# Kernel tuning notes

Hardware: AMD Instinct MI355X
Metric: run time of the kernel (lower is better)

Reference implementation:

```python
import jax, jax.numpy as jnp
import numpy as np

H = 8
HD = 16  # head_dim = out_features // n_heads = 128 // 8


def setup_inputs() -> dict:
    key = jax.random.key(0)
    k1, k2, k3, k4, k5 = jax.random.split(key, 5)
    B, N, F_IN, F_OUT = 4, 2048, 128, 128
    x = jax.random.normal(k1, (B, N, F_IN), dtype=jnp.float32)
    adj = jax.random.randint(k2, (B, N, N), 0, 2, dtype=jnp.int32)
    W = jax.random.normal(k3, (F_IN, F_OUT), dtype=jnp.float32) * (1.0 / np.sqrt(F_IN))
    a = jax.random.normal(k4, (H, 2 * HD), dtype=jnp.float32) * 0.1
    Wo = jax.random.normal(k5, (F_OUT, F_OUT), dtype=jnp.float32) * (1.0 / np.sqrt(F_OUT))
    bo = jnp.zeros((F_OUT,), dtype=jnp.float32)
    return {"x": x, "adj": adj, "W": W, "a": a, "Wo": Wo, "bo": bo}


def reference(x, adj, W, a, Wo, bo):
    B, N, _ = x.shape
    # Linear projection (no bias), split heads: [B,H,N,HD]
    Wx = (x @ W).reshape(B, N, H, HD).transpose(0, 2, 1, 3)
    # Additive attention scores: e_ij = leaky(a_l . Wx_i + a_r . Wx_j)
    e_i = jnp.einsum('bhnd,hd->bhn', Wx, a[:, :HD])  # [B,H,N]
    e_j = jnp.einsum('bhnd,hd->bhn', Wx, a[:, HD:])  # [B,H,N]
    e = jax.nn.leaky_relu(e_i[:, :, :, None] + e_j[:, :, None, :], negative_slope=0.2)
    # Mask to edges of adj; rows with no edges -> all -inf -> softmax NaN -> 0
    mask = (adj[:, None, :, :] == 0)  # [B,1,N,N] broadcast over heads
    e = jnp.where(mask, -jnp.inf, e)
    attn = jax.nn.softmax(e, axis=-1)
    attn = jnp.nan_to_num(attn, nan=0.0)
    # Weighted aggregation, merge heads: [B,N,F_OUT]
    h = jnp.einsum('bhij,bhjd->bhid', attn, Wx)
    h = h.transpose(0, 2, 1, 3).reshape(B, N, H * HD)
    # out_proj (nn.Linear: y = h @ Wo.T + bo) then ELU
    return jax.nn.elu(h @ Wo.T + bo)
```

## Files before the change

### kernel.cpp

```cpp
#include <hip/hip_runtime.h>
#include <hip/hip_bf16.h>
#include <cstdint>


typedef float f32x2 __attribute__((ext_vector_type(2)));
typedef float f32x4 __attribute__((ext_vector_type(4)));
typedef __bf16 bf16x8 __attribute__((ext_vector_type(8)));
typedef unsigned long long u64;

__device__ __forceinline__ float lsel(float v, u64 m, u64 lanebit) {
#if __has_builtin(__builtin_amdgcn_inverse_ballot_w64)
    (void)lanebit;
    return __builtin_amdgcn_inverse_ballot_w64(m) ? v : 0.0f;
#else
    return (m & lanebit) ? v : 0.0f;
#endif
}

__global__ __launch_bounds__(256)
void prep_kernel(const float* __restrict__ x, const float* __restrict__ W,
                 const float* __restrict__ a, const float* __restrict__ Wo,
                 const int* __restrict__ adj,
                 unsigned short* __restrict__ wxT,
                 float2* __restrict__ EI,
                 float* __restrict__ EjT, float* __restrict__ Ej5T,
                 float* __restrict__ WoT,
                 u64* __restrict__ tmask)
{
    const int t = threadIdx.x;

    if (blockIdx.x < 2048) {
        __shared__ int al[16][257];
        const int blk2 = blockIdx.x;
        const int b = blk2 >> 9;
        const int tile = (blk2 >> 2) & 127;
        const int jq = blk2 & 3;
        const int rowbase = b * 2048 + tile * 16;
        const int w = t >> 6, lane = t & 63;
        const int r = lane & 15, jg = lane >> 4;
        const int srow = t >> 4, scol = (t & 15) * 16;

        #pragma unroll
        for (int cc = 0; cc < 2; ++cc) {
            const int jc = jq * 512 + cc * 256;
            const int* gsrc = adj + (size_t)(rowbase + srow) * 2048 + jc + scol;
            #pragma unroll
            for (int q = 0; q < 4; ++q) {
                const int4 v = *reinterpret_cast<const int4*>(&gsrc[q * 4]);
                al[srow][scol + q * 4 + 0] = v.x;
                al[srow][scol + q * 4 + 1] = v.y;
                al[srow][scol + q * 4 + 2] = v.z;
                al[srow][scol + q * 4 + 3] = v.w;
            }
            __syncthreads();
            u64 myw = 0;
            #pragma unroll
            for (int kk = 0; kk < 2; ++kk) {
                const int c0 = w * 64 + kk * 32 + jg * 8;
                const int4 a0 = *reinterpret_cast<const int4*>(&al[r][c0]);
                const int4 a1 = *reinterpret_cast<const int4*>(&al[r][c0 + 4]);
                const int av[8] = {a0.x, a0.y, a0.z, a0.w, a1.x, a1.y, a1.z, a1.w};
                #pragma unroll
                for (int e = 0; e < 8; ++e) {
                    const u64 bal = __ballot(av[e] != 0);
                    const int widx = kk * 8 + e;
                    if (lane == widx) myw = bal;
                }
            }
            __syncthreads();
            const int jtw = jq * 8 + cc * 4 + w;
            if (lane < 16)
                tmask[((size_t)(b * 128 + tile) * 32 + jtw) * 16 + lane] = myw;
        }
        return;
    }

    const int blk = blockIdx.x - 2048;
    if (blk == 1024) {
        if (t < 128)
            for (int k = 0; k < 128; ++k)
                WoT[k * 128 + t] = Wo[t * 128 + k];
        return;
    }
    __shared__ float xl[8 * 128];
    __shared__ float xw[8 * 128];
    const int row0 = blk * 8;
    if (t < 128) {
        #pragma unroll
        for (int r = 0; r < 8; ++r)
            xl[r * 128 + t] = x[(size_t)(row0 + r) * 128 + t];
    }
    __syncthreads();

    if (t < 128) {
        float acc[8] = {0.f, 0.f, 0.f, 0.f, 0.f, 0.f, 0.f, 0.f};
        for (int k = 0; k < 128; k += 4) {
            const float w0 = W[(k + 0) * 128 + t];
            const float w1 = W[(k + 1) * 128 + t];
            const float w2 = W[(k + 2) * 128 + t];
            const float w3 = W[(k + 3) * 128 + t];
            #pragma unroll
            for (int r = 0; r < 8; ++r) {
                const float4 xv = *reinterpret_cast<const float4*>(&xl[r * 128 + k]);
                acc[r] += xv.x * w0 + xv.y * w1 + xv.z * w2 + xv.w * w3;
            }
        }
        #pragma unroll
        for (int r = 0; r < 8; ++r) xw[r * 128 + t] = acc[r];
    }
    __syncthreads();

    if (t < 128) {
        const int b = row0 >> 11, n0 = row0 & 2047;
        bf16x8 st;
        #pragma unroll
        for (int r = 0; r < 8; ++r) st[r] = (__bf16)xw[r * 128 + t];
        *reinterpret_cast<bf16x8*>(&wxT[((size_t)(b * 128 + t)) * 2048 + n0]) = st;

        const int r = t >> 4, h = (t >> 1) & 7, s = t & 1;
        float dot = 0.f;
        #pragma unroll
        for (int d = 0; d < 16; ++d)
            dot += xw[r * 128 + h * 16 + d] * a[h * 32 + s * 16 + d];
        const float ef  = __expf(dot);
        const float ef5 = __expf(0.2f * dot);
        const int idx = (b * 8 + h) * 2048 + n0 + r;
        if (s) { EjT[idx] = ef; Ej5T[idx] = ef5; }
        else   { float2 ev; ev.x = ef; ev.y = ef5; EI[idx] = ev; }
    }
}

__global__ __launch_bounds__(256)
void vshuf_kernel(const unsigned short* __restrict__ wxT,
                  unsigned short* __restrict__ vfrag)
{
    const int gid = blockIdx.x * 256 + threadIdx.x;
    const int lane = gid & 63;
    const int w32 = (gid >> 6) & 63;
    const int bh = gid >> 12;
    const int b = bh >> 3, h = bh & 7;
    const int f = h * 16 + (lane & 15);
    const int j = w32 * 32 + (lane >> 4) * 8;
    const bf16x8 v = *reinterpret_cast<const bf16x8*>(
        &wxT[((size_t)(b * 128 + f)) * 2048 + j]);
    *reinterpret_cast<bf16x8*>(&vfrag[(size_t)gid * 8]) = v;
}

__global__ __launch_bounds__(512, 4)
void gat_kernel(const u64* __restrict__ tmask,
                const unsigned short* __restrict__ vfrag,
                const float2* __restrict__ EI,
                const float* __restrict__ EjT, const float* __restrict__ Ej5T,
                const float* __restrict__ WoT, const float* __restrict__ bo,
                float* __restrict__ out)
{
    const int tid = threadIdx.x;
    const int h = tid >> 6;
    const int lane = tid & 63;
    const int r = lane & 15;
    const int jg = lane >> 4;
    const int jaof = jg * 8;
    const u64 lanebit = 1ull << lane;
    const int bid = (blockIdx.x & 7) * 64 + (blockIdx.x >> 3);
    const int b = bid >> 7;
    const int tile = bid & 127;
    const int ibase = tile << 4;

    __shared__ __align__(16) float EjL[2][8][128];
    __shared__ __align__(16) float Ej5L[2][8][128];
    __shared__ float hacc[16][128];

    const int eb = (b * 8 + h) * 2048;
    const float2 q0 = EI[eb + ibase + r];
    f32x2 EiE, Ei5E;
    EiE[0] = q0.x; EiE[1] = q0.x; Ei5E[0] = q0.y; Ei5E[1] = q0.y;
    const u64* tmrow = tmask + (size_t)(b * 128 + tile) * 512;

    const unsigned short* vfr = vfrag + (size_t)(b * 8 + h) * 64 * 64 * 8;
    const int jj = lane;
    const float* EjG  = EjT  + eb;
    const float* Ej5G = Ej5T + eb;

    f32x4 acc  = {0.f, 0.f, 0.f, 0.f};
    f32x4 accS = {0.f, 0.f, 0.f, 0.f};
    bf16x8 ones;
    #pragma unroll
    for (int e2 = 0; e2 < 8; ++e2) ones[e2] = (__bf16)1.0f;

    bf16x8 vC0, vC1, vC2, vC3, vN0, vN1, vN2, vN3;
    vC0 = *reinterpret_cast<const bf16x8*>(&vfr[(0 * 64 + lane) * 8]);
    vC1 = *reinterpret_cast<const bf16x8*>(&vfr[(1 * 64 + lane) * 8]);
    vC2 = *reinterpret_cast<const bf16x8*>(&vfr[(2 * 64 + lane) * 8]);
    vC3 = *reinterpret_cast<const bf16x8*>(&vfr[(3 * 64 + lane) * 8]);
    {
        const float2 s0 = *reinterpret_cast<const float2*>(&EjG[jj * 2]);
        const float2 s1 = *reinterpret_cast<const float2*>(&Ej5G[jj * 2]);
        *reinterpret_cast<float2*>(&EjL[0][h][jj * 2]) = s0;
        *reinterpret_cast<float2*>(&Ej5L[0][h][jj * 2]) = s1;
    }
    __syncthreads();

    int cur = 0;
    for (int c = 0; c < 16; ++c) {
        const int cn = (c + 1) & 15;
        const int w32n = cn * 4;
        const int jn = (c + 1) * 128;
        vN0 = *reinterpret_cast<const bf16x8*>(&vfr[((w32n + 0) * 64 + lane) * 8]);
        vN1 = *reinterpret_cast<const bf16x8*>(&vfr[((w32n + 1) * 64 + lane) * 8]);
        vN2 = *reinterpret_cast<const bf16x8*>(&vfr[((w32n + 2) * 64 + lane) * 8]);
        vN3 = *reinterpret_cast<const bf16x8*>(&vfr[((w32n + 3) * 64 + lane) * 8]);
        const float2 sn  = *reinterpret_cast<const float2*>(&EjG[jn + jj * 2]);
        const float2 sn5 = *reinterpret_cast<const float2*>(&Ej5G[jn + jj * 2]);
        __builtin_amdgcn_sched_barrier(0);

        const u64* tmw = tmrow + c * 32;
        u64 mwA[16], mwB[16];
        #pragma unroll
        for (int e2 = 0; e2 < 16; ++e2) mwA[e2] = tmw[e2];
        #pragma unroll
        for (int e2 = 0; e2 < 16; ++e2) mwB[e2] = tmw[16 + e2];

        #pragma unroll
        for (int kk = 0; kk < 4; ++kk) {
            const int jloc = kk * 32 + jaof;
            const float4 e0 = *reinterpret_cast<const float4*>(&EjL[cur][h][jloc]);
            const float4 e1 = *reinterpret_cast<const float4*>(&EjL[cur][h][jloc + 4]);
            const float4 f0 = *reinterpret_cast<const float4*>(&Ej5L[cur][h][jloc]);
            const float4 f1 = *reinterpret_cast<const float4*>(&Ej5L[cur][h][jloc + 4]);
            const bf16x8 v = (kk == 0) ? vC0 : (kk == 1) ? vC1 : (kk == 2) ? vC2 : vC3;
            const u64* mwp = (kk < 2) ? mwA : mwB;
            const int mof = (kk & 1) * 8;
            bf16x8 afr;
            #pragma unroll
            for (int ep = 0; ep < 4; ++ep) {
                const float4 ejv = (ep & 2) ? e1 : e0;
                const float4 ej5 = (ep & 2) ? f1 : f0;
                f32x2 ejp, ej5p;
                if (ep & 1) { ejp[0]=ejv.z; ejp[1]=ejv.w; ej5p[0]=ej5.z; ej5p[1]=ej5.w; }
                else        { ejp[0]=ejv.x; ejp[1]=ejv.y; ej5p[0]=ej5.x; ej5p[1]=ej5.y; }
                const f32x2 t1 = EiE * ejp;
                const f32x2 t2 = Ei5E * ej5p;
#if __has_builtin(__builtin_elementwise_max)
                const f32x2 tm2 = __builtin_elementwise_max(t1, t2);
#else
                f32x2 tm2; tm2[0] = fmaxf(t1[0], t2[0]); tm2[1] = fmaxf(t1[1], t2[1]);
#endif
                afr[2 * ep]     = (__bf16)lsel(tm2[0], mwp[mof + 2 * ep],     lanebit);
                afr[2 * ep + 1] = (__bf16)lsel(tm2[1], mwp[mof + 2 * ep + 1], lanebit);
            }
            acc  = __builtin_amdgcn_mfma_f32_16x16x32_bf16(afr, v,    acc,  0, 0, 0);
            accS = __builtin_amdgcn_mfma_f32_16x16x32_bf16(afr, ones, accS, 0, 0, 0);
        }

        const int nb = cur ^ 1;
        *reinterpret_cast<float2*>(&EjL[nb][h][jj * 2]) = sn;
        *reinterpret_cast<float2*>(&Ej5L[nb][h][jj * 2]) = sn5;
        __syncthreads();
        vC0 = vN0; vC1 = vN1; vC2 = vN2; vC3 = vN3;
        cur = nb;
    }

    #pragma unroll
    for (int q = 0; q < 4; ++q) {
        const int row = jg * 4 + q;
        const float inv = (accS[q] > 0.f) ? 1.f / accS[q] : 0.f;
        hacc[row][h * 16 + r] = acc[q] * inv;
    }
    __syncthreads();

    const int f = tid & 127;
    const int rg = tid >> 7;
    float o0 = 0.f, o1 = 0.f, o2 = 0.f, o3 = 0.f;
    for (int k = 0; k < 128; k += 4) {
        const float w0 = WoT[(k + 0) * 128 + f];
        const float w1 = WoT[(k + 1) * 128 + f];
        const float w2 = WoT[(k + 2) * 128 + f];
        const float w3 = WoT[(k + 3) * 128 + f];
        const float4 h0 = *reinterpret_cast<const float4*>(&hacc[rg * 4 + 0][k]);
        const float4 h1 = *reinterpret_cast<const float4*>(&hacc[rg * 4 + 1][k]);
        const float4 h2v = *reinterpret_cast<const float4*>(&hacc[rg * 4 + 2][k]);
        const float4 h3 = *reinterpret_cast<const float4*>(&hacc[rg * 4 + 3][k]);
        o0 += h0.x * w0 + h0.y * w1 + h0.z * w2 + h0.w * w3;
        o1 += h1.x * w0 + h1.y * w1 + h1.z * w2 + h1.w * w3;
        o2 += h2v.x * w0 + h2v.y * w1 + h2v.z * w2 + h2v.w * w3;
        o3 += h3.x * w0 + h3.y * w1 + h3.z * w2 + h3.w * w3;
    }
    const float bv = bo[f];
    float vv[4] = {o0 + bv, o1 + bv, o2 + bv, o3 + bv};
    #pragma unroll
    for (int q = 0; q < 4; ++q) {
        float v = vv[q];
        v = (v > 0.f) ? v : (__expf(v) - 1.f);
        out[(size_t)(b * 2048 + ibase + rg * 4 + q) * 128 + f] = v;
    }
}

extern "C" void kernel_launch(void* const* d_in, const int* in_sizes, int n_in,
                              void* d_out, int out_size, void* d_ws, size_t ws_size,
                              hipStream_t stream) {
    const float* x   = (const float*)d_in[0];
    const int*   adj = (const int*)d_in[1];
    const float* W   = (const float*)d_in[2];
    const float* a   = (const float*)d_in[3];
    const float* Wo  = (const float*)d_in[4];
    const float* bo  = (const float*)d_in[5];
    float* out = (float*)d_out;

    char* ws = (char*)d_ws;
    unsigned short* wxT = (unsigned short*)ws;
    float2* EI  = (float2*)(ws + (size_t)2 * 1024 * 1024);
    float* EjT  = (float*)(EI + 4 * 8 * 2048);
    float* Ej5T = EjT + 4 * 8 * 2048;
    float* WoT  = Ej5T + 4 * 8 * 2048;
    u64* tmask = (u64*)(WoT + 128 * 128);
    unsigned short* vfrag = (unsigned short*)(tmask + (size_t)512 * 512);

    prep_kernel<<<dim3(2048 + 1025), dim3(256), 0, stream>>>(
        x, W, a, Wo, adj, wxT, EI, EjT, Ej5T, WoT, tmask);
    vshuf_kernel<<<dim3(512), dim3(256), 0, stream>>>(wxT, vfrag);
    gat_kernel<<<dim3(512), dim3(512), 0, stream>>>(
        tmask, vfrag, EI, EjT, Ej5T, WoT, bo, out);
}
```

Before: 72.28 us.

## Split GAT blocks by head group, interleave Ej arrays, separate out-projection kernel

```diff
diff --git a/kernel.cpp b/kernel.cpp
--- a/kernel.cpp
+++ b/kernel.cpp
@@ -22,60 +22,55 @@
                  const float* __restrict__ a, const float* __restrict__ Wo,
                  const int* __restrict__ adj,
                  unsigned short* __restrict__ wxT,
-                 float2* __restrict__ EI,
-                 float* __restrict__ EjT, float* __restrict__ Ej5T,
+                 float2* __restrict__ EI, float2* __restrict__ EJ2,
                  float* __restrict__ WoT,
                  u64* __restrict__ tmask)
 {
     const int t = threadIdx.x;
 
-    if (blockIdx.x < 2048) {
+    if (blockIdx.x < 4096) {
         __shared__ int al[16][257];
         const int blk2 = blockIdx.x;
-        const int b = blk2 >> 9;
-        const int tile = (blk2 >> 2) & 127;
-        const int jq = blk2 & 3;
+        const int b = blk2 >> 10;
+        const int tile = (blk2 >> 3) & 127;
+        const int jcc = blk2 & 7;
+        const int jc = jcc * 256;
         const int rowbase = b * 2048 + tile * 16;
         const int w = t >> 6, lane = t & 63;
         const int r = lane & 15, jg = lane >> 4;
         const int srow = t >> 4, scol = (t & 15) * 16;
 
-        #pragma unroll
-        for (int cc = 0; cc < 2; ++cc) {
-            const int jc = jq * 512 + cc * 256;
-            const int* gsrc = adj + (size_t)(rowbase + srow) * 2048 + jc + scol;
+        const int* gsrc = adj + (size_t)(rowbase + srow) * 2048 + jc + scol;
+        #pragma unroll
+        for (int q = 0; q < 4; ++q) {
+            const int4 v = *reinterpret_cast<const int4*>(&gsrc[q * 4]);
+            al[srow][scol + q * 4 + 0] = v.x;
+            al[srow][scol + q * 4 + 1] = v.y;
+            al[srow][scol + q * 4 + 2] = v.z;
+            al[srow][scol + q * 4 + 3] = v.w;
+        }
+        __syncthreads();
+        u64 myw = 0;
+        #pragma unroll
+        for (int kk = 0; kk < 2; ++kk) {
+            const int c0 = w * 64 + kk * 32 + jg * 8;
+            const int4 a0 = *reinterpret_cast<const int4*>(&al[r][c0]);
+            const int4 a1 = *reinterpret_cast<const int4*>(&al[r][c0 + 4]);
+            const int av[8] = {a0.x, a0.y, a0.z, a0.w, a1.x, a1.y, a1.z, a1.w};
             #pragma unroll
-            for (int q = 0; q < 4; ++q) {
-                const int4 v = *reinterpret_cast<const int4*>(&gsrc[q * 4]);
-                al[srow][scol + q * 4 + 0] = v.x;
-                al[srow][scol + q * 4 + 1] = v.y;
-                al[srow][scol + q * 4 + 2] = v.z;
-                al[srow][scol + q * 4 + 3] = v.w;
+            for (int e = 0; e < 8; ++e) {
+                const u64 bal = __ballot(av[e] != 0);
+                const int widx = kk * 8 + e;
+                if (lane == widx) myw = bal;
             }
-            __syncthreads();
-            u64 myw = 0;
-            #pragma unroll
-            for (int kk = 0; kk < 2; ++kk) {
-                const int c0 = w * 64 + kk * 32 + jg * 8;
-                const int4 a0 = *reinterpret_cast<const int4*>(&al[r][c0]);
-                const int4 a1 = *reinterpret_cast<const int4*>(&al[r][c0 + 4]);
-                const int av[8] = {a0.x, a0.y, a0.z, a0.w, a1.x, a1.y, a1.z, a1.w};
-                #pragma unroll
-                for (int e = 0; e < 8; ++e) {
-                    const u64 bal = __ballot(av[e] != 0);
-                    const int widx = kk * 8 + e;
-                    if (lane == widx) myw = bal;
-                }
-            }
-            __syncthreads();
-            const int jtw = jq * 8 + cc * 4 + w;
-            if (lane < 16)
-                tmask[((size_t)(b * 128 + tile) * 32 + jtw) * 16 + lane] = myw;
-        }
+        }
+        const int jtw = jcc * 4 + w;
+        if (lane < 16)
+            tmask[((size_t)(b * 128 + tile) * 32 + jtw) * 16 + lane] = myw;
         return;
     }
 
-    const int blk = blockIdx.x - 2048;
+    const int blk = blockIdx.x - 4096;
     if (blk == 1024) {
         if (t < 128)
             for (int k = 0; k < 128; ++k)
@@ -122,11 +117,9 @@
         #pragma unroll
         for (int d = 0; d < 16; ++d)
             dot += xw[r * 128 + h * 16 + d] * a[h * 32 + s * 16 + d];
-        const float ef  = __expf(dot);
-        const float ef5 = __expf(0.2f * dot);
+        float2 ev; ev.x = __expf(dot); ev.y = __expf(0.2f * dot);
         const int idx = (b * 8 + h) * 2048 + n0 + r;
-        if (s) { EjT[idx] = ef; Ej5T[idx] = ef5; }
-        else   { float2 ev; ev.x = ef; ev.y = ef5; EI[idx] = ev; }
+        if (s) EJ2[idx] = ev; else EI[idx] = ev;
     }
 }
 
@@ -146,40 +139,35 @@
     *reinterpret_cast<bf16x8*>(&vfrag[(size_t)gid * 8]) = v;
 }
 
-__global__ __launch_bounds__(512, 4)
+__global__ __launch_bounds__(256, 8)
 void gat_kernel(const u64* __restrict__ tmask,
                 const unsigned short* __restrict__ vfrag,
-                const float2* __restrict__ EI,
-                const float* __restrict__ EjT, const float* __restrict__ Ej5T,
-                const float* __restrict__ WoT, const float* __restrict__ bo,
-                float* __restrict__ out)
+                const float2* __restrict__ EI, const float2* __restrict__ EJ2,
+                float* __restrict__ hnorm)
 {
     const int tid = threadIdx.x;
-    const int h = tid >> 6;
+    const int hw = tid >> 6;
     const int lane = tid & 63;
     const int r = lane & 15;
     const int jg = lane >> 4;
     const int jaof = jg * 8;
     const u64 lanebit = 1ull << lane;
-    const int bid = (blockIdx.x & 7) * 64 + (blockIdx.x >> 3);
-    const int b = bid >> 7;
-    const int tile = bid & 127;
+    const int bid = (blockIdx.x & 7) * 128 + (blockIdx.x >> 3);
+    const int tg = bid >> 1;
+    const int hg = bid & 1;
+    const int b = tg >> 7;
+    const int tile = tg & 127;
     const int ibase = tile << 4;
-
-    __shared__ __align__(16) float EjL[2][8][128];
-    __shared__ __align__(16) float Ej5L[2][8][128];
-    __shared__ float hacc[16][128];
+    const int h = hg * 4 + hw;
+
+    __shared__ __align__(16) float2 EjL[2][4][128];
 
     const int eb = (b * 8 + h) * 2048;
     const float2 q0 = EI[eb + ibase + r];
-    f32x2 EiE, Ei5E;
-    EiE[0] = q0.x; EiE[1] = q0.x; Ei5E[0] = q0.y; Ei5E[1] = q0.y;
+    f32x2 Eipk; Eipk[0] = q0.x; Eipk[1] = q0.y;
     const u64* tmrow = tmask + (size_t)(b * 128 + tile) * 512;
-
     const unsigned short* vfr = vfrag + (size_t)(b * 8 + h) * 64 * 64 * 8;
-    const int jj = lane;
-    const float* EjG  = EjT  + eb;
-    const float* Ej5G = Ej5T + eb;
+    const float2* EJ2G = EJ2 + eb;
 
     f32x4 acc  = {0.f, 0.f, 0.f, 0.f};
     f32x4 accS = {0.f, 0.f, 0.f, 0.f};
@@ -193,24 +181,20 @@
     vC2 = *reinterpret_cast<const bf16x8*>(&vfr[(2 * 64 + lane) * 8]);
     vC3 = *reinterpret_cast<const bf16x8*>(&vfr[(3 * 64 + lane) * 8]);
     {
-        const float2 s0 = *reinterpret_cast<const float2*>(&EjG[jj * 2]);
-        const float2 s1 = *reinterpret_cast<const float2*>(&Ej5G[jj * 2]);
-        *reinterpret_cast<float2*>(&EjL[0][h][jj * 2]) = s0;
-        *reinterpret_cast<float2*>(&Ej5L[0][h][jj * 2]) = s1;
+        const float4 s0 = *reinterpret_cast<const float4*>(&EJ2G[lane * 2]);
+        *reinterpret_cast<float4*>(&EjL[0][hw][lane * 2]) = s0;
     }
     __syncthreads();
 
     int cur = 0;
     for (int c = 0; c < 16; ++c) {
-        const int cn = (c + 1) & 15;
-        const int w32n = cn * 4;
+        const int w32n = ((c + 1) & 15) * 4;
         const int jn = (c + 1) * 128;
         vN0 = *reinterpret_cast<const bf16x8*>(&vfr[((w32n + 0) * 64 + lane) * 8]);
         vN1 = *reinterpret_cast<const bf16x8*>(&vfr[((w32n + 1) * 64 + lane) * 8]);
         vN2 = *reinterpret_cast<const bf16x8*>(&vfr[((w32n + 2) * 64 + lane) * 8]);
         vN3 = *reinterpret_cast<const bf16x8*>(&vfr[((w32n + 3) * 64 + lane) * 8]);
-        const float2 sn  = *reinterpret_cast<const float2*>(&EjG[jn + jj * 2]);
-        const float2 sn5 = *reinterpret_cast<const float2*>(&Ej5G[jn + jj * 2]);
+        const float4 snq = *reinterpret_cast<const float4*>(&EJ2G[jn + lane * 2]);
         __builtin_amdgcn_sched_barrier(0);
 
         const u64* tmw = tmrow + c * 32;
@@ -222,39 +206,26 @@
 
         #pragma unroll
         for (int kk = 0; kk < 4; ++kk) {
-            const int jloc = kk * 32 + jaof;
-            const float4 e0 = *reinterpret_cast<const float4*>(&EjL[cur][h][jloc]);
-            const float4 e1 = *reinterpret_cast<const float4*>(&EjL[cur][h][jloc + 4]);
-            const float4 f0 = *reinterpret_cast<const float4*>(&Ej5L[cur][h][jloc]);
-            const float4 f1 = *reinterpret_cast<const float4*>(&Ej5L[cur][h][jloc + 4]);
+            const float2* ejp = &EjL[cur][hw][kk * 32 + jaof];
             const bf16x8 v = (kk == 0) ? vC0 : (kk == 1) ? vC1 : (kk == 2) ? vC2 : vC3;
             const u64* mwp = (kk < 2) ? mwA : mwB;
             const int mof = (kk & 1) * 8;
             bf16x8 afr;
             #pragma unroll
-            for (int ep = 0; ep < 4; ++ep) {
-                const float4 ejv = (ep & 2) ? e1 : e0;
-                const float4 ej5 = (ep & 2) ? f1 : f0;
-                f32x2 ejp, ej5p;
-                if (ep & 1) { ejp[0]=ejv.z; ejp[1]=ejv.w; ej5p[0]=ej5.z; ej5p[1]=ej5.w; }
-                else        { ejp[0]=ejv.x; ejp[1]=ejv.y; ej5p[0]=ej5.x; ej5p[1]=ej5.y; }
-                const f32x2 t1 = EiE * ejp;
-                const f32x2 t2 = Ei5E * ej5p;
-#if __has_builtin(__builtin_elementwise_max)
-                const f32x2 tm2 = __builtin_elementwise_max(t1, t2);
-#else
-                f32x2 tm2; tm2[0] = fmaxf(t1[0], t2[0]); tm2[1] = fmaxf(t1[1], t2[1]);
-#endif
-                afr[2 * ep]     = (__bf16)lsel(tm2[0], mwp[mof + 2 * ep],     lanebit);
-                afr[2 * ep + 1] = (__bf16)lsel(tm2[1], mwp[mof + 2 * ep + 1], lanebit);
+            for (int e2 = 0; e2 < 8; ++e2) {
+                const float2 q = ejp[e2];
+                f32x2 tq; tq[0] = q.x; tq[1] = q.y;
+                const f32x2 tt = Eipk * tq;
+                const float p = fmaxf(tt[0], tt[1]);
+                afr[e2] = (__bf16)lsel(p, mwp[mof + e2], lanebit);
             }
             acc  = __builtin_amdgcn_mfma_f32_16x16x32_bf16(afr, v,    acc,  0, 0, 0);
             accS = __builtin_amdgcn_mfma_f32_16x16x32_bf16(afr, ones, accS, 0, 0, 0);
         }
 
         const int nb = cur ^ 1;
-        *reinterpret_cast<float2*>(&EjL[nb][h][jj * 2]) = sn;
-        *reinterpret_cast<float2*>(&Ej5L[nb][h][jj * 2]) = sn5;
+        *reinterpret_cast<float4*>(&EjL[nb][hw][lane * 2]) =
+            *reinterpret_cast<const float4*>(&snq);
         __syncthreads();
         vC0 = vN0; vC1 = vN1; vC2 = vN2; vC3 = vN3;
         cur = nb;
@@ -264,34 +235,49 @@
     for (int q = 0; q < 4; ++q) {
         const int row = jg * 4 + q;
         const float inv = (accS[q] > 0.f) ? 1.f / accS[q] : 0.f;
-        hacc[row][h * 16 + r] = acc[q] * inv;
+        hnorm[(size_t)(b * 2048 + ibase + row) * 128 + h * 16 + r] = acc[q] * inv;
+    }
+}
+
+__global__ __launch_bounds__(256)
+void outproj_kernel(const float* __restrict__ hnorm, const float* __restrict__ WoT,
+                    const float* __restrict__ bo, float* __restrict__ out)
+{
+    const int tid = threadIdx.x;
+    const int bid = (blockIdx.x & 7) * 64 + (blockIdx.x >> 3);
+    const int b = bid >> 7;
+    const int tile = bid & 127;
+    const int ibase = tile << 4;
+
+    __shared__ float hl[16][128];
+    const float* src = hnorm + (size_t)(b * 2048 + ibase) * 128;
+    #pragma unroll
+    for (int k = 0; k < 8; ++k) {
+        const int idx = k * 256 + tid;
+        hl[idx >> 7][idx & 127] = src[idx];
     }
     __syncthreads();
 
     const int f = tid & 127;
     const int rg = tid >> 7;
-    float o0 = 0.f, o1 = 0.f, o2 = 0.f, o3 = 0.f;
+    float o[8] = {0.f, 0.f, 0.f, 0.f, 0.f, 0.f, 0.f, 0.f};
     for (int k = 0; k < 128; k += 4) {
         const float w0 = WoT[(k + 0) * 128 + f];
         const float w1 = WoT[(k + 1) * 128 + f];
         const float w2 = WoT[(k + 2) * 128 + f];
         const float w3 = WoT[(k + 3) * 128 + f];
-        const float4 h0 = *reinterpret_cast<const float4*>(&hacc[rg * 4 + 0][k]);
-        const float4 h1 = *reinterpret_cast<const float4*>(&hacc[rg * 4 + 1][k]);
-        const float4 h2v = *reinterpret_cast<const float4*>(&hacc[rg * 4 + 2][k]);
-        const float4 h3 = *reinterpret_cast<const float4*>(&hacc[rg * 4 + 3][k]);
-        o0 += h0.x * w0 + h0.y * w1 + h0.z * w2 + h0.w * w3;
-        o1 += h1.x * w0 + h1.y * w1 + h1.z * w2 + h1.w * w3;
-        o2 += h2v.x * w0 + h2v.y * w1 + h2v.z * w2 + h2v.w * w3;
-        o3 += h3.x * w0 + h3.y * w1 + h3.z * w2 + h3.w * w3;
+        #pragma unroll
+        for (int q = 0; q < 8; ++q) {
+            const float4 hv = *reinterpret_cast<const float4*>(&hl[rg * 8 + q][k]);
+            o[q] += hv.x * w0 + hv.y * w1 + hv.z * w2 + hv.w * w3;
+        }
     }
     const float bv = bo[f];
-    float vv[4] = {o0 + bv, o1 + bv, o2 + bv, o3 + bv};
     #pragma unroll
-    for (int q = 0; q < 4; ++q) {
-        float v = vv[q];
+    for (int q = 0; q < 8; ++q) {
+        float v = o[q] + bv;
         v = (v > 0.f) ? v : (__expf(v) - 1.f);
-        out[(size_t)(b * 2048 + ibase + rg * 4 + q) * 128 + f] = v;
+        out[(size_t)(b * 2048 + ibase + rg * 8 + q) * 128 + f] = v;
     }
 }
 
@@ -309,15 +295,16 @@
     char* ws = (char*)d_ws;
     unsigned short* wxT = (unsigned short*)ws;
     float2* EI  = (float2*)(ws + (size_t)2 * 1024 * 1024);
-    float* EjT  = (float*)(EI + 4 * 8 * 2048);
-    float* Ej5T = EjT + 4 * 8 * 2048;
-    float* WoT  = Ej5T + 4 * 8 * 2048;
+    float2* EJ2 = EI + 4 * 8 * 2048;
+    float* WoT  = (float*)(EJ2 + 4 * 8 * 2048);
     u64* tmask = (u64*)(WoT + 128 * 128);
     unsigned short* vfrag = (unsigned short*)(tmask + (size_t)512 * 512);
-
-    prep_kernel<<<dim3(2048 + 1025), dim3(256), 0, stream>>>(
-        x, W, a, Wo, adj, wxT, EI, EjT, Ej5T, WoT, tmask);
+    float* hnorm = (float*)(vfrag + (size_t)1024 * 1024);
+
+    prep_kernel<<<dim3(4096 + 1025), dim3(256), 0, stream>>>(
+        x, W, a, Wo, adj, wxT, EI, EJ2, WoT, tmask);
     vshuf_kernel<<<dim3(512), dim3(256), 0, stream>>>(wxT, vfrag);
-    gat_kernel<<<dim3(512), dim3(512), 0, stream>>>(
-        tmask, vfrag, EI, EjT, Ej5T, WoT, bo, out);
-}
+    gat_kernel<<<dim3(1024), dim3(256), 0, stream>>>(
+        tmask, vfrag, EI, EJ2, hnorm);
+    outproj_kernel<<<dim3(512), dim3(256), 0, stream>>>(hnorm, WoT, bo, out);
+}
```

Result: slower. 99.45 us (+37.6%).
